# Kernel tuning notes

Hardware: AMD Instinct MI355X
Metric: run time of the kernel (lower is better)

## Reference

```python
import jax, jax.numpy as jnp
import numpy as np

HIDDEN, LATENT, SYM, BOX = 512, 256, 64, 128
LEAF = 16384
NODE = 2 * LEAF - 1  # 32767: complete binary tree, leaves first
W_SCALE = 0.05  # keep tanh unsaturated


def setup_inputs() -> dict:
    key = jax.random.key(0)
    ks = jax.random.split(key, 16)
    # kids: valid tree structure (randint per-spec would give invalid child pointers).
    # Leaves are nodes [0, LEAF); internal node LEAF+j merges nodes 2j and 2j+1
    # (1-indexed pointers 2j+1, 2j+2). Every 4th internal node is a symmetry node.
    j = np.arange(NODE - LEAF)
    kids = np.zeros((1, NODE, 3), dtype=np.int32)
    kids[0, LEAF:, 0] = 2 * j + 1
    kids[0, LEAF:, 1] = 2 * j + 2
    kids[0, LEAF:, 2] = (j % 4 == 3).astype(np.int32)
    f32 = jnp.float32
    return {
        "kids": jnp.asarray(kids),
        "shape": jax.random.normal(ks[0], (1, BOX, LEAF), dtype=f32),
        "param": jax.random.normal(ks[1], (1, NODE, SYM), dtype=f32),
        # leaf / box encoder: box -> latent
        "Wb": jax.random.normal(ks[2], (BOX, LATENT), dtype=f32) * W_SCALE,
        "bb": jnp.zeros((LATENT,), dtype=f32),
        # adjacency encoder: (latent, latent) -> hidden -> latent
        "Wl": jax.random.normal(ks[3], (LATENT, HIDDEN), dtype=f32) * W_SCALE,
        "Wr": jax.random.normal(ks[4], (LATENT, HIDDEN), dtype=f32) * W_SCALE,
        "b1": jnp.zeros((HIDDEN,), dtype=f32),
        "W2": jax.random.normal(ks[5], (HIDDEN, LATENT), dtype=f32) * W_SCALE,
        "b2": jnp.zeros((LATENT,), dtype=f32),
        # symmetry encoder: (latent, sym) -> hidden -> latent
        "Wsl": jax.random.normal(ks[6], (LATENT, HIDDEN), dtype=f32) * W_SCALE,
        "Wsr": jax.random.normal(ks[7], (SYM, HIDDEN), dtype=f32) * W_SCALE,
        "bs1": jnp.zeros((HIDDEN,), dtype=f32),
        "Ws2": jax.random.normal(ks[8], (HIDDEN, LATENT), dtype=f32) * W_SCALE,
        "bs2": jnp.zeros((LATENT,), dtype=f32),
    }


def reference(kids, shape, param, Wb, bb, Wl, Wr, b1, W2, b2, Wsl, Wsr, bs1, Ws2, bs2):
    nodeNum = kids.shape[1]
    leafNum = shape.shape[2]
    latent = Wb.shape[1]

    # Leaves (nodes 0..leafNum-1, kids[...,0]==0) have no data dependence on hOut:
    # encode them all at once. boxes: [leafNum, box]
    boxes = jnp.transpose(shape[0])
    hLeaf = jnp.tanh(boxes @ Wb + bb)  # [leafNum, latent]
    hOut = jnp.zeros((nodeNum, latent), dtype=shape.dtype).at[:leafNum].set(hLeaf)

    p = param[0]  # [nodeNum, sym]
    k = kids[0]   # [nodeNum, 3]

    def step(h, x):
        i, k0, k1, k2 = x
        a = h[k0 - 1]      # [latent] left child hidden
        b = h[k1 - 1]      # [latent] right child hidden (adjacency case)
        s = p[k0 - 1]      # [sym]    (source indexes param with kids[...,0]-1)
        # adjacency merge
        h1 = jnp.tanh(jnp.tanh(a @ Wl + b @ Wr + b1) @ W2 + b2)
        # symmetry merge
        h2 = jnp.tanh(jnp.tanh(a @ Wsl + s @ Wsr + bs1) @ Ws2 + bs2)
        hi = jnp.where(k2 == 1, h2, h1)
        return h.at[i].set(hi), None

    # internal nodes are i in [leafNum, nodeNum); original only defines inputs there
    idx = jnp.arange(leafNum, nodeNum)
    xs = (idx, k[leafNum:, 0], k[leafNum:, 1], k[leafNum:, 2])
    hOut, _ = jax.lax.scan(step, hOut, xs)
    return hOut[nodeNum - 1][None, :]  # [1, latent], the root code
```

## Files before the change

kernel.cpp:

```cpp
#include <hip/hip_runtime.h>

#define LEAF   16384
#define NNODE  (2*LEAF-1)
#define LATENT 256
#define HIDDEN 512
#define SYM    64
#define BOX    128

using half8 = __attribute__((ext_vector_type(8))) _Float16;
using f32x4 = __attribute__((ext_vector_type(4))) float;

__device__ __forceinline__ f32x4 mfma16h(half8 a, half8 b, f32x4 c){
    return __builtin_amdgcn_mfma_f32_16x16x32_f16(a, b, c, 0, 0, 0);
}

__global__ void pack_all(const float* __restrict__ Wl, const float* __restrict__ Wr,
                         const float* __restrict__ Wsl, const float* __restrict__ Wsr,
                         const float* __restrict__ W2, const float* __restrict__ Ws2,
                         const float* __restrict__ Wb,
                         _Float16* __restrict__ wcat, _Float16* __restrict__ wscat,
                         _Float16* __restrict__ w2p, _Float16* __restrict__ ws2p,
                         _Float16* __restrict__ wbp)
{
    int g = blockIdx.x*256 + threadIdx.x;
    const float *A, *B; _Float16* pk; int Ksplit, N, KS, t;
    if (g < 262144)      { t = g;          A=Wl;  B=Wr;  pk=wcat;  Ksplit=256; N=512; KS=16; }
    else if (g < 425984) { t = g-262144;   A=Wsl; B=Wsr; pk=wscat; Ksplit=256; N=512; KS=10; }
    else if (g < 557056) { t = g-425984;   A=W2;  B=W2;  pk=w2p;   Ksplit=512; N=256; KS=16; }
    else if (g < 688128) { t = g-557056;   A=Ws2; B=Ws2; pk=ws2p;  Ksplit=512; N=256; KS=16; }
    else if (g < 720896) { t = g-688128;   A=Wb;  B=Wb;  pk=wbp;   Ksplit=128; N=256; KS=4;  }
    else return;
    int j = t & 7, l = (t>>3)&63, tile = (t>>9)&3;
    int rest = t >> 11;
    int ks = rest % KS, cb = rest / KS;
    int k   = ks*32 + ((l>>4)*8) + j;
    int col = cb*64 + tile*16 + (l&15);
    float wv = (k < Ksplit) ? A[(size_t)k*N + col] : B[(size_t)(k-Ksplit)*N + col];
    pk[((size_t)(cb*KS + ks)*4 + tile)*512 + (size_t)l*8 + j] = (_Float16)wv;
}

__global__ __launch_bounds__(256) void leaf_mfma_kernel(
    const float* __restrict__ shape, const _Float16* __restrict__ wbpk,
    const float* __restrict__ bb, _Float16* __restrict__ hh)
{
    const int t = threadIdx.x, lane = t & 63, w = t >> 6;
    const int r0 = blockIdx.x * 64;
    const int m = r0 + w*16 + (lane & 15);

    half8 A[4];
    #pragma unroll
    for (int ks = 0; ks < 4; ++ks) {
        #pragma unroll
        for (int e = 0; e < 8; ++e) {
            int k = ks*32 + (lane >> 4)*8 + e;
            A[ks][e] = (_Float16)shape[(size_t)k*LEAF + m];
        }
    }

    for (int cb = 0; cb < 4; ++cb) {
        f32x4 acc[4];
        #pragma unroll
        for (int c = 0; c < 4; ++c) acc[c] = (f32x4){0.f,0.f,0.f,0.f};
        #pragma unroll
        for (int ks = 0; ks < 4; ++ks) {
            const _Float16* pb = wbpk + (size_t)((cb*4 + ks)*4)*512;
            #pragma unroll
            for (int tile = 0; tile < 4; ++tile) {
                half8 B = *(const half8*)(pb + tile*512 + lane*8);
                acc[tile] = mfma16h(A[ks], B, acc[tile]);
            }
        }
        #pragma unroll
        for (int tile = 0; tile < 4; ++tile) {
            int col = cb*64 + tile*16 + (lane & 15);
            float bv = bb[col];
            #pragma unroll
            for (int r = 0; r < 4; ++r) {
                int row = r0 + w*16 + (lane >> 4)*4 + r;
                hh[(size_t)row*256 + col] = (_Float16)tanhf(acc[tile][r] + bv);
            }
        }
    }
}

template<int NSUB>
__device__ __forceinline__ void k1_body(
    int rb, int cb, int start, int n,
    const _Float16* __restrict__ hh, const float* __restrict__ param,
    const _Float16* __restrict__ wcatpk, const _Float16* __restrict__ wscatpk,
    const float* __restrict__ b1, const float* __restrict__ bs1,
    _Float16* __restrict__ U, _Float16* __restrict__ V)
{
    __shared__ __align__(16) _Float16 ldsB1[2*2048];
    const int t = threadIdx.x, lane = t & 63, w = t >> 6;
    const bool isV = cb >= 8;
    const int cbl = isV ? cb - 8 : cb;
    const int KS  = isV ? 10 : 16;
    const _Float16* pk = (isV ? wscatpk : wcatpk) + (size_t)cbl * KS * 2048;
    const int row0  = rb * NSUB * 64;
    const int cbase = 2 * (start - LEAF);

    f32x4 acc[NSUB][4];
    #pragma unroll
    for (int s = 0; s < NSUB; ++s)
        #pragma unroll
        for (int c = 0; c < 4; ++c) acc[s][c] = (f32x4){0.f,0.f,0.f,0.f};

    *(half8*)(ldsB1 + t*8) = *(const half8*)(pk + (size_t)t*8);
    __syncthreads();

    for (int ks = 0; ks < KS; ++ks) {
        const bool hasNext = ks + 1 < KS;
        half8 stg;
        if (hasNext) stg = *(const half8*)(pk + (size_t)(ks+1)*2048 + (size_t)t*8);
        half8 A[NSUB];
        #pragma unroll
        for (int s = 0; s < NSUB; ++s) {
            int m = row0 + (s*4 + w)*16 + (lane & 15);
            if (m >= n) m = n - 1;
            if (!isV || ks < 8) {
                int node = cbase + 2*m + (ks >= 8 ? 1 : 0);
                A[s] = *(const half8*)(hh + (size_t)node*256 + (size_t)(ks & 7)*32 + ((lane >> 4)*8));
            } else {
                const float* pp = param + (size_t)(cbase + 2*m)*64 + (ks - 8)*32 + (lane >> 4)*8;
                float4 p0 = *(const float4*)pp;
                float4 p1 = *(const float4*)(pp + 4);
                A[s][0]=(_Float16)p0.x; A[s][1]=(_Float16)p0.y; A[s][2]=(_Float16)p0.z; A[s][3]=(_Float16)p0.w;
                A[s][4]=(_Float16)p1.x; A[s][5]=(_Float16)p1.y; A[s][6]=(_Float16)p1.z; A[s][7]=(_Float16)p1.w;
            }
        }
        const _Float16* lb = ldsB1 + (ks & 1)*2048;
        #pragma unroll
        for (int tile = 0; tile < 4; ++tile) {
            half8 Bh = *(const half8*)(lb + tile*512 + lane*8);
            #pragma unroll
            for (int s = 0; s < NSUB; ++s)
                acc[s][tile] = mfma16h(A[s], Bh, acc[s][tile]);
        }
        if (hasNext)
            *(half8*)(ldsB1 + ((ks+1) & 1)*2048 + t*8) = stg;
        __syncthreads();
    }

    const float* bias = isV ? bs1 : b1;
    _Float16* o = isV ? V : U;
    #pragma unroll
    for (int s = 0; s < NSUB; ++s) {
        #pragma unroll
        for (int tile = 0; tile < 4; ++tile) {
            int col = cbl*64 + tile*16 + (lane & 15);
            float bv = bias[col];
            #pragma unroll
            for (int r = 0; r < 4; ++r) {
                int m = row0 + (s*4 + w)*16 + (lane >> 4)*4 + r;
                if (m < n)
                    o[(size_t)m*512 + col] = (_Float16)tanhf(acc[s][tile][r] + bv);
            }
        }
    }
}

template<int NSUB>
__device__ __forceinline__ void k2_body(
    int rb, int cb, int start, int n,
    const _Float16* __restrict__ U, const _Float16* __restrict__ V,
    const int* __restrict__ kids,
    const _Float16* __restrict__ w2pk, const _Float16* __restrict__ ws2pk,
    const float* __restrict__ b2, const float* __restrict__ bs2,
    _Float16* __restrict__ hh)
{
    __shared__ __align__(16) _Float16 ldsB2[2*2048];
    const int t = threadIdx.x, lane = t & 63, w = t >> 6;
    const bool isSym = cb >= 4;
    const int cbl = isSym ? cb - 4 : cb;
    const _Float16* pk = (isSym ? ws2pk : w2pk) + (size_t)cbl * 16 * 2048;
    const _Float16* Asrc = isSym ? V : U;
    const int row0 = rb * NSUB * 64;

    f32x4 acc[NSUB][4];
    #pragma unroll
    for (int s = 0; s < NSUB; ++s)
        #pragma unroll
        for (int c = 0; c < 4; ++c) acc[s][c] = (f32x4){0.f,0.f,0.f,0.f};

    *(half8*)(ldsB2 + t*8) = *(const half8*)(pk + (size_t)t*8);
    __syncthreads();

    for (int ks = 0; ks < 16; ++ks) {
        const bool hasNext = ks + 1 < 16;
        half8 stg;
        if (hasNext) stg = *(const half8*)(pk + (size_t)(ks+1)*2048 + (size_t)t*8);
        half8 A[NSUB];
        #pragma unroll
        for (int s = 0; s < NSUB; ++s) {
            int m = row0 + (s*4 + w)*16 + (lane & 15);
            if (m >= n) m = n - 1;
            A[s] = *(const half8*)(Asrc + (size_t)m*512 + (size_t)ks*32 + ((lane >> 4)*8));
        }
        const _Float16* lb = ldsB2 + (ks & 1)*2048;
        #pragma unroll
        for (int tile = 0; tile < 4; ++tile) {
            half8 Bh = *(const half8*)(lb + tile*512 + lane*8);
            #pragma unroll
            for (int s = 0; s < NSUB; ++s)
                acc[s][tile] = mfma16h(A[s], Bh, acc[s][tile]);
        }
        if (hasNext)
            *(half8*)(ldsB2 + ((ks+1) & 1)*2048 + t*8) = stg;
        __syncthreads();
    }

    const float* bias = isSym ? bs2 : b2;
    const int want = isSym ? 1 : 0;
    #pragma unroll
    for (int s = 0; s < NSUB; ++s) {
        #pragma unroll
        for (int tile = 0; tile < 4; ++tile) {
            int col = cbl*64 + tile*16 + (lane & 15);
            float bv = bias[col];
            #pragma unroll
            for (int r = 0; r < 4; ++r) {
                int m = row0 + (s*4 + w)*16 + (lane >> 4)*4 + r;
                if (m < n && kids[3*(start + m) + 2] == want)
                    hh[(size_t)(start + m)*256 + col] = (_Float16)tanhf(acc[s][tile][r] + bv);
            }
        }
    }
}

template<int NSUB>
__global__ __launch_bounds__(256) void k1_kernel(
    const _Float16* __restrict__ hh, const float* __restrict__ param,
    const _Float16* __restrict__ wcatpk, const _Float16* __restrict__ wscatpk,
    const float* __restrict__ b1, const float* __restrict__ bs1,
    _Float16* __restrict__ U, _Float16* __restrict__ V, int start, int n)
{
    k1_body<NSUB>(blockIdx.x, blockIdx.y, start, n, hh, param, wcatpk, wscatpk, b1, bs1, U, V);
}

template<int NSUB>
__global__ __launch_bounds__(256) void k2_kernel(
    const _Float16* __restrict__ U, const _Float16* __restrict__ V,
    const int* __restrict__ kids,
    const _Float16* __restrict__ w2pk, const _Float16* __restrict__ ws2pk,
    const float* __restrict__ b2, const float* __restrict__ bs2,
    _Float16* __restrict__ hh, int start, int n)
{
    k2_body<NSUB>(blockIdx.x, blockIdx.y, start, n, U, V, kids, w2pk, ws2pk, b2, bs2, hh);
}

__device__ __forceinline__ void k1_tail(
    int rb, int cb, int start, int n,
    const _Float16* __restrict__ hh, const float* __restrict__ param,
    const _Float16* wlds,
    const float* __restrict__ b1, const float* __restrict__ bs1,
    _Float16* __restrict__ U, _Float16* __restrict__ V)
{
    const int t = threadIdx.x, lane = t & 63, w = t >> 6;
    const bool isV = cb >= 8;
    const int cbl = isV ? cb - 8 : cb;
    const int KS  = isV ? 10 : 16;
    const int row0  = rb * 64;
    const int cbase = 2 * (start - LEAF);

    f32x4 acc[4];
    #pragma unroll
    for (int c = 0; c < 4; ++c) acc[c] = (f32x4){0.f,0.f,0.f,0.f};

    int m = row0 + w*16 + (lane & 15);
    if (m >= n) m = n - 1;

    for (int ks = 0; ks < KS; ++ks) {
        half8 A;
        if (!isV || ks < 8) {
            int node = cbase + 2*m + (ks >= 8 ? 1 : 0);
            A = *(const half8*)(hh + (size_t)node*256 + (size_t)(ks & 7)*32 + ((lane >> 4)*8));
        } else {
            const float* pp = param + (size_t)(cbase + 2*m)*64 + (ks - 8)*32 + (lane >> 4)*8;
            float4 p0 = *(const float4*)pp;
            float4 p1 = *(const float4*)(pp + 4);
            A[0]=(_Float16)p0.x; A[1]=(_Float16)p0.y; A[2]=(_Float16)p0.z; A[3]=(_Float16)p0.w;
            A[4]=(_Float16)p1.x; A[5]=(_Float16)p1.y; A[6]=(_Float16)p1.z; A[7]=(_Float16)p1.w;
        }
        const _Float16* lb = wlds + ks*2048;
        #pragma unroll
        for (int tile = 0; tile < 4; ++tile) {
            half8 Bh = *(const half8*)(lb + tile*512 + lane*8);
            acc[tile] = mfma16h(A, Bh, acc[tile]);
        }
    }

    const float* bias = isV ? bs1 : b1;
    _Float16* o = isV ? V : U;
    #pragma unroll
    for (int tile = 0; tile < 4; ++tile) {
        int col = cbl*64 + tile*16 + (lane & 15);
        float bv = bias[col];
        #pragma unroll
        for (int r = 0; r < 4; ++r) {
            int mm = row0 + w*16 + (lane >> 4)*4 + r;
            if (mm < n)
                o[(size_t)mm*512 + col] = (_Float16)tanhf(acc[tile][r] + bv);
        }
    }
}

__device__ __forceinline__ void k2_tail(
    int rb, int cb, int start, int n,
    const _Float16* __restrict__ U, const _Float16* __restrict__ V,
    const int* __restrict__ kids,
    const _Float16* wlds,
    const float* __restrict__ b2, const float* __restrict__ bs2,
    _Float16* __restrict__ hh)
{
    const int t = threadIdx.x, lane = t & 63, w = t >> 6;
    const bool isSym = cb >= 4;
    const int cbl = isSym ? cb - 4 : cb;
    const _Float16* Asrc = isSym ? V : U;
    const int row0 = rb * 64;

    f32x4 acc[4];
    #pragma unroll
    for (int c = 0; c < 4; ++c) acc[c] = (f32x4){0.f,0.f,0.f,0.f};

    int m = row0 + w*16 + (lane & 15);
    if (m >= n) m = n - 1;

    for (int ks = 0; ks < 16; ++ks) {
        half8 A = *(const half8*)(Asrc + (size_t)m*512 + (size_t)ks*32 + ((lane >> 4)*8));
        const _Float16* lb = wlds + ks*2048;
        #pragma unroll
        for (int tile = 0; tile < 4; ++tile) {
            half8 Bh = *(const half8*)(lb + tile*512 + lane*8);
            acc[tile] = mfma16h(A, Bh, acc[tile]);
        }
    }

    const float* bias = isSym ? bs2 : b2;
    const int want = isSym ? 1 : 0;
    #pragma unroll
    for (int tile = 0; tile < 4; ++tile) {
        int col = cbl*64 + tile*16 + (lane & 15);
        float bv = bias[col];
        #pragma unroll
        for (int r = 0; r < 4; ++r) {
            int mm = row0 + w*16 + (lane >> 4)*4 + r;
            if (mm < n && kids[3*(start + mm) + 2] == want)
                hh[(size_t)(start + mm)*256 + col] = (_Float16)tanhf(acc[tile][r] + bv);
        }
    }
}

#define TAILG 96
__device__ __forceinline__ void fbar(unsigned* flags, unsigned tgt)
{
    __syncthreads();
    if (threadIdx.x == 0)
        __hip_atomic_store(flags + blockIdx.x*16, tgt, __ATOMIC_RELEASE, __HIP_MEMORY_SCOPE_AGENT);
    if (threadIdx.x < TAILG) {
        while (__hip_atomic_load(flags + threadIdx.x*16, __ATOMIC_RELAXED, __HIP_MEMORY_SCOPE_AGENT) < tgt)
            __builtin_amdgcn_s_sleep(1);
    }
    __syncthreads();
    __builtin_amdgcn_fence(__ATOMIC_ACQUIRE, "agent");
}

__global__ __launch_bounds__(256) void tail_kernel(
    _Float16* __restrict__ hh, const float* __restrict__ param,
    const _Float16* __restrict__ wcatpk, const _Float16* __restrict__ wscatpk,
    const float* __restrict__ b1, const float* __restrict__ bs1,
    _Float16* __restrict__ U, _Float16* __restrict__ V,
    const int* __restrict__ kids,
    const _Float16* __restrict__ w2pk, const _Float16* __restrict__ ws2pk,
    const float* __restrict__ b2, const float* __restrict__ bs2,
    unsigned* __restrict__ flags, float* __restrict__ out)
{
    __shared__ __align__(16) _Float16 wlds[16*2048];
    const int b = blockIdx.x;
    const int t = threadIdx.x;
    const bool isK1 = b < 64;
    int cb, rh;
    const _Float16* src;
    int nh;
    if (isK1) {
        cb = b & 15; rh = b >> 4;
        if (cb < 8) { src = wcatpk  + (size_t)cb*16*2048;     nh = 16*256; }
        else        { src = wscatpk + (size_t)(cb-8)*10*2048; nh = 10*256; }
    } else {
        int i = b - 64; cb = i & 7; rh = i >> 3;
        if (cb < 4) src = w2pk  + (size_t)cb*16*2048;
        else        src = ws2pk + (size_t)(cb-4)*16*2048;
        nh = 16*256;
    }
    for (int i = t; i < nh; i += 256)
        *(half8*)(wlds + (size_t)i*8) = *(const half8*)(src + (size_t)i*8);
    __syncthreads();

    unsigned tgt = 0;
    int start = LEAF + 8192 + 4096 + 2048;
    for (int n = 1024; n >= 1; n >>= 1) {
        int rt = (n + 63) >> 6;
        if (isK1) {
            for (int r = rh; r < rt; r += 4)
                k1_tail(r, cb, start, n, hh, param, wlds, b1, bs1, U, V);
        }
        ++tgt; fbar(flags, tgt);
        if (!isK1) {
            for (int r = rh; r < rt; r += 4)
                k2_tail(r, cb, start, n, U, V, kids, wlds, b2, bs2, hh);
        }
        ++tgt; fbar(flags, tgt);
        start += n;
    }
    if (b == 0)
        out[t] = (float)hh[(size_t)(NNODE - 1)*256 + t];
}

extern "C" void kernel_launch(void* const* d_in, const int* in_sizes, int n_in,
                              void* d_out, int out_size, void* d_ws, size_t ws_size,
                              hipStream_t stream) {
    const int*   kids  = (const int*)  d_in[0];
    const float* shape = (const float*)d_in[1];
    const float* param = (const float*)d_in[2];
    const float* Wb    = (const float*)d_in[3];
    const float* bb    = (const float*)d_in[4];
    const float* Wl    = (const float*)d_in[5];
    const float* Wr    = (const float*)d_in[6];
    const float* b1    = (const float*)d_in[7];
    const float* W2    = (const float*)d_in[8];
    const float* b2    = (const float*)d_in[9];
    const float* Wsl   = (const float*)d_in[10];
    const float* Wsr   = (const float*)d_in[11];
    const float* bs1   = (const float*)d_in[12];
    const float* Ws2   = (const float*)d_in[13];
    const float* bs2   = (const float*)d_in[14];
    float* out = (float*)d_out;

    char* ws = (char*)d_ws;
    _Float16* hh      = (_Float16*)(ws + 0);
    _Float16* U       = (_Float16*)(ws + 16777216);
    _Float16* V       = (_Float16*)(ws + 25165824);
    _Float16* wcatpk  = (_Float16*)(ws + 33554432);
    _Float16* wscatpk = (_Float16*)(ws + 34078720);
    _Float16* w2pk    = (_Float16*)(ws + 34406400);
    _Float16* ws2pk   = (_Float16*)(ws + 34668544);
    _Float16* wbpk    = (_Float16*)(ws + 34930688);
    unsigned* flags   = (unsigned*)(ws + 34996224);

    hipMemsetAsync(flags, 0, TAILG*64, stream);

    pack_all<<<2816, 256, 0, stream>>>(Wl, Wr, Wsl, Wsr, W2, Ws2, Wb,
                                       wcatpk, wscatpk, w2pk, ws2pk, wbpk);

    leaf_mfma_kernel<<<LEAF/64, 256, 0, stream>>>(shape, wbpk, bb, hh);

    int start = LEAF;
    for (int n = 8192; n >= 2048; n >>= 1) {
        if (n == 8192) {
            k1_kernel<2><<<dim3(n/128, 16), 256, 0, stream>>>(hh, param, wcatpk, wscatpk,
                                                              b1, bs1, U, V, start, n);
        } else {
            k1_kernel<1><<<dim3(n/64, 16), 256, 0, stream>>>(hh, param, wcatpk, wscatpk,
                                                             b1, bs1, U, V, start, n);
        }
        k2_kernel<1><<<dim3(n/64, 8), 256, 0, stream>>>(U, V, kids, w2pk, ws2pk,
                                                        b2, bs2, hh, start, n);
        start += n;
    }

    tail_kernel<<<TAILG, 256, 0, stream>>>(hh, param, wcatpk, wscatpk, b1, bs1,
                                           U, V, kids, w2pk, ws2pk, b2, bs2, flags, out);
}
```

Baseline: 416.4 us.

## Shrink persistent tail kernel and move levels 1024/512 to regular launches

The persistent tail kernel now runs with 48 blocks instead of 96 and starts at the level with 256 nodes. The 1024 and 512 levels go back to separate k1/k2 kernel launches. This makes each flag barrier cheaper, since it polls fewer blocks, in exchange for two extra launches and less parallelism in the tail. Bias values are now preloaded into registers once per block, and global loads and stores in the tail bodies are marked nontemporal.

```diff
diff --git a/kernel.cpp b/kernel.cpp
--- a/kernel.cpp
+++ b/kernel.cpp
@@ -252,8 +252,7 @@
 __device__ __forceinline__ void k1_tail(
     int rb, int cb, int start, int n,
     const _Float16* __restrict__ hh, const float* __restrict__ param,
-    const _Float16* wlds,
-    const float* __restrict__ b1, const float* __restrict__ bs1,
+    const _Float16* wlds, f32x4 bv,
     _Float16* __restrict__ U, _Float16* __restrict__ V)
 {
     const int t = threadIdx.x, lane = t & 63, w = t >> 6;
@@ -274,13 +273,14 @@
         half8 A;
         if (!isV || ks < 8) {
             int node = cbase + 2*m + (ks >= 8 ? 1 : 0);
-            A = *(const half8*)(hh + (size_t)node*256 + (size_t)(ks & 7)*32 + ((lane >> 4)*8));
+            A = __builtin_nontemporal_load(
+                (const half8*)(hh + (size_t)node*256 + (size_t)(ks & 7)*32 + ((lane >> 4)*8)));
         } else {
             const float* pp = param + (size_t)(cbase + 2*m)*64 + (ks - 8)*32 + (lane >> 4)*8;
-            float4 p0 = *(const float4*)pp;
-            float4 p1 = *(const float4*)(pp + 4);
-            A[0]=(_Float16)p0.x; A[1]=(_Float16)p0.y; A[2]=(_Float16)p0.z; A[3]=(_Float16)p0.w;
-            A[4]=(_Float16)p1.x; A[5]=(_Float16)p1.y; A[6]=(_Float16)p1.z; A[7]=(_Float16)p1.w;
+            f32x4 p0 = __builtin_nontemporal_load((const f32x4*)pp);
+            f32x4 p1 = __builtin_nontemporal_load((const f32x4*)(pp + 4));
+            A[0]=(_Float16)p0[0]; A[1]=(_Float16)p0[1]; A[2]=(_Float16)p0[2]; A[3]=(_Float16)p0[3];
+            A[4]=(_Float16)p1[0]; A[5]=(_Float16)p1[1]; A[6]=(_Float16)p1[2]; A[7]=(_Float16)p1[3];
         }
         const _Float16* lb = wlds + ks*2048;
         #pragma unroll
@@ -290,17 +290,16 @@
         }
     }
 
-    const float* bias = isV ? bs1 : b1;
     _Float16* o = isV ? V : U;
     #pragma unroll
     for (int tile = 0; tile < 4; ++tile) {
         int col = cbl*64 + tile*16 + (lane & 15);
-        float bv = bias[col];
         #pragma unroll
         for (int r = 0; r < 4; ++r) {
             int mm = row0 + w*16 + (lane >> 4)*4 + r;
             if (mm < n)
-                o[(size_t)mm*512 + col] = (_Float16)tanhf(acc[tile][r] + bv);
+                __builtin_nontemporal_store(
+                    (_Float16)tanhf(acc[tile][r] + bv[tile]), o + (size_t)mm*512 + col);
         }
     }
 }
@@ -309,8 +308,7 @@
     int rb, int cb, int start, int n,
     const _Float16* __restrict__ U, const _Float16* __restrict__ V,
     const int* __restrict__ kids,
-    const _Float16* wlds,
-    const float* __restrict__ b2, const float* __restrict__ bs2,
+    const _Float16* wlds, f32x4 bv,
     _Float16* __restrict__ hh)
 {
     const int t = threadIdx.x, lane = t & 63, w = t >> 6;
@@ -327,7 +325,8 @@
     if (m >= n) m = n - 1;
 
     for (int ks = 0; ks < 16; ++ks) {
-        half8 A = *(const half8*)(Asrc + (size_t)m*512 + (size_t)ks*32 + ((lane >> 4)*8));
+        half8 A = __builtin_nontemporal_load(
+            (const half8*)(Asrc + (size_t)m*512 + (size_t)ks*32 + ((lane >> 4)*8)));
         const _Float16* lb = wlds + ks*2048;
         #pragma unroll
         for (int tile = 0; tile < 4; ++tile) {
@@ -336,22 +335,24 @@
         }
     }
 
-    const float* bias = isSym ? bs2 : b2;
     const int want = isSym ? 1 : 0;
     #pragma unroll
     for (int tile = 0; tile < 4; ++tile) {
         int col = cbl*64 + tile*16 + (lane & 15);
-        float bv = bias[col];
         #pragma unroll
         for (int r = 0; r < 4; ++r) {
             int mm = row0 + w*16 + (lane >> 4)*4 + r;
-            if (mm < n && kids[3*(start + mm) + 2] == want)
-                hh[(size_t)(start + mm)*256 + col] = (_Float16)tanhf(acc[tile][r] + bv);
-        }
-    }
-}
-
-#define TAILG 96
+            if (mm < n) {
+                int k2v = __builtin_nontemporal_load(kids + 3*(start + mm) + 2);
+                if (k2v == want)
+                    __builtin_nontemporal_store(
+                        (_Float16)tanhf(acc[tile][r] + bv[tile]), hh + (size_t)(start + mm)*256 + col);
+            }
+        }
+    }
+}
+
+#define TAILG 48
 __device__ __forceinline__ void fbar(unsigned* flags, unsigned tgt)
 {
     __syncthreads();
@@ -377,37 +378,46 @@
 {
     __shared__ __align__(16) _Float16 wlds[16*2048];
     const int b = blockIdx.x;
-    const int t = threadIdx.x;
-    const bool isK1 = b < 64;
+    const int t = threadIdx.x, lane = t & 63;
+    const bool isK1 = b < 32;
     int cb, rh;
     const _Float16* src;
+    const float* bias;
     int nh;
     if (isK1) {
         cb = b & 15; rh = b >> 4;
-        if (cb < 8) { src = wcatpk  + (size_t)cb*16*2048;     nh = 16*256; }
-        else        { src = wscatpk + (size_t)(cb-8)*10*2048; nh = 10*256; }
+        if (cb < 8) { src = wcatpk  + (size_t)cb*16*2048;     nh = 16*256; bias = b1; }
+        else        { src = wscatpk + (size_t)(cb-8)*10*2048; nh = 10*256; bias = bs1; }
     } else {
-        int i = b - 64; cb = i & 7; rh = i >> 3;
-        if (cb < 4) src = w2pk  + (size_t)cb*16*2048;
-        else        src = ws2pk + (size_t)(cb-4)*16*2048;
+        int i = b - 32; cb = i & 7; rh = i >> 3;
+        if (cb < 4) { src = w2pk  + (size_t)cb*16*2048;     bias = b2; }
+        else        { src = ws2pk + (size_t)(cb-4)*16*2048; bias = bs2; }
         nh = 16*256;
     }
     for (int i = t; i < nh; i += 256)
         *(half8*)(wlds + (size_t)i*8) = *(const half8*)(src + (size_t)i*8);
+
+    f32x4 bv;
+    {
+        int cbl = isK1 ? (cb & 7) : (cb & 3);
+        #pragma unroll
+        for (int tile = 0; tile < 4; ++tile)
+            bv[tile] = bias[cbl*64 + tile*16 + (lane & 15)];
+    }
     __syncthreads();
 
     unsigned tgt = 0;
-    int start = LEAF + 8192 + 4096 + 2048;
-    for (int n = 1024; n >= 1; n >>= 1) {
+    int start = LEAF + 8192 + 4096 + 2048 + 1024 + 512;
+    for (int n = 256; n >= 1; n >>= 1) {
         int rt = (n + 63) >> 6;
         if (isK1) {
-            for (int r = rh; r < rt; r += 4)
-                k1_tail(r, cb, start, n, hh, param, wlds, b1, bs1, U, V);
+            for (int r = rh; r < rt; r += 2)
+                k1_tail(r, cb, start, n, hh, param, wlds, bv, U, V);
         }
         ++tgt; fbar(flags, tgt);
         if (!isK1) {
-            for (int r = rh; r < rt; r += 4)
-                k2_tail(r, cb, start, n, U, V, kids, wlds, b2, bs2, hh);
+            for (int r = rh; r < rt; r += 2)
+                k2_tail(r, cb, start, n, U, V, kids, wlds, bv, hh);
         }
         ++tgt; fbar(flags, tgt);
         start += n;
@@ -455,7 +465,7 @@
     leaf_mfma_kernel<<<LEAF/64, 256, 0, stream>>>(shape, wbpk, bb, hh);
 
     int start = LEAF;
-    for (int n = 8192; n >= 2048; n >>= 1) {
+    for (int n = 8192; n >= 512; n >>= 1) {
         if (n == 8192) {
             k1_kernel<2><<<dim3(n/128, 16), 256, 0, stream>>>(hh, param, wcatpk, wscatpk,
                                                               b1, bs1, U, V, start, n);
```

Result: faster. 400.1 us (-3.9%).
